# Optimization experiments

Hardware: AMD Instinct MI355X
Metric: run time of the kernel (lower is better)

## Reference

```python
import jax, jax.numpy as jnp
import numpy as np

INPUT_DIM = 8192
OUTPUT_DIM = 16384
SPARSITY = 0.02
TOP_K = int(SPARSITY * OUTPUT_DIM)  # 327


def setup_inputs() -> dict:
    key = jax.random.key(0)
    kx, kp = jax.random.split(key)
    # Binary SDR input, batch of 1 (the layer hard-codes batch=1 in its sparse output)
    x = jax.random.randint(kx, (1, INPUT_DIM), 0, 2, dtype=jnp.int32)
    # Permanence weights ~ U[0, 1), as in tf.random_uniform in build()
    p = jax.random.uniform(kp, (INPUT_DIM, OUTPUT_DIM), dtype=jnp.float32)
    return {"x": x, "p": p}


def reference(x, p):
    # connection = round(permanence) -> binary {0,1} int32 connectivity matrix
    connection = jnp.round(p).astype(jnp.int32)
    # overlap: int32 binarized GEMV, [1, OUTPUT_DIM]
    overlap = jnp.matmul(x, connection)
    # top-k winner columns (unsorted in tf; index set is identical)
    _, act_indices = jax.lax.top_k(overlap[0], TOP_K)
    # Dense equivalent of SparseTensor(indices, ones, [1, OUTPUT_DIM])
    activation = jnp.zeros((1, OUTPUT_DIM), dtype=jnp.float32).at[0, act_indices].set(1.0)
    return activation
```

## Files before the change

### kernel.cpp

```cpp
#include <hip/hip_runtime.h>
#include <hip/hip_bf16.h>

#define IN_DIM 8192
#define OUT_DIM 16384
#define K_TOP 327

__global__ void zero_kernel(int* __restrict__ overlap) {
    int i = blockIdx.x * blockDim.x + threadIdx.x;
    if (i < OUT_DIM) overlap[i] = 0;
}

__global__ __launch_bounds__(256) void overlap_kernel(const int* __restrict__ x,
                                                      const float* __restrict__ p,
                                                      int* __restrict__ overlap) {
    constexpr int ROWS = 128;
    __shared__ int rows[ROWS];
    __shared__ int nact_sh;
    const int tid = threadIdx.x;
    const int row0 = blockIdx.y * ROWS;

    if (tid == 0) nact_sh = 0;
    __syncthreads();
    if (tid < ROWS) {
        if (x[row0 + tid] != 0) {
            int idx = atomicAdd(&nact_sh, 1);
            rows[idx] = tid;
        }
    }
    __syncthreads();
    const int n = nact_sh;

    const int col = blockIdx.x * 1024 + tid * 4;
    const float* pc = p + col;
    int a0 = 0, a1 = 0, a2 = 0, a3 = 0;

    int k = 0;
    for (; k + 1 < n; k += 2) {
        int r1 = rows[k], r2 = rows[k + 1];
        float4 v1 = *(const float4*)(pc + (size_t)(row0 + r1) * OUT_DIM);
        float4 v2 = *(const float4*)(pc + (size_t)(row0 + r2) * OUT_DIM);
        a0 += (v1.x > 0.5f) + (v2.x > 0.5f);
        a1 += (v1.y > 0.5f) + (v2.y > 0.5f);
        a2 += (v1.z > 0.5f) + (v2.z > 0.5f);
        a3 += (v1.w > 0.5f) + (v2.w > 0.5f);
    }
    if (k < n) {
        int r1 = rows[k];
        float4 v1 = *(const float4*)(pc + (size_t)(row0 + r1) * OUT_DIM);
        a0 += (v1.x > 0.5f);
        a1 += (v1.y > 0.5f);
        a2 += (v1.z > 0.5f);
        a3 += (v1.w > 0.5f);
    }
    atomicAdd(&overlap[col + 0], a0);
    atomicAdd(&overlap[col + 1], a1);
    atomicAdd(&overlap[col + 2], a2);
    atomicAdd(&overlap[col + 3], a3);
}

__device__ __forceinline__ int block_scan_incl(int val, int tid, int* wsums) {
    const int lane = tid & 63;
    const int wave = tid >> 6;
    int v = val;
#pragma unroll
    for (int d = 1; d < 64; d <<= 1) {
        int nv = __shfl_up(v, d, 64);
        if (lane >= d) v += nv;
    }
    if (lane == 63) wsums[wave] = v;
    __syncthreads();
    if (wave == 0) {
        int w = (lane < 16) ? wsums[lane] : 0;
#pragma unroll
        for (int d = 1; d < 16; d <<= 1) {
            int nw = __shfl_up(w, d, 64);
            if (lane >= d) w += nw;
        }
        if (lane < 16) wsums[lane] = w;
    }
    __syncthreads();
    int offset = (wave > 0) ? wsums[wave - 1] : 0;
    return v + offset;
}

#define NB 9216
__global__ __launch_bounds__(1024) void topk_kernel(const int* __restrict__ overlap,
                                                    float* __restrict__ out) {
    __shared__ int hist[NB];
    __shared__ int wsums[16];
    __shared__ int sh_T;
    __shared__ int sh_R;
    const int tid = threadIdx.x;

    for (int i = tid; i < NB; i += 1024) hist[i] = 0;
    if (tid == 0) sh_T = -1;
    __syncthreads();

    int ov_local[16];
#pragma unroll
    for (int c = 0; c < 16; ++c) {
        int ov = overlap[c * 1024 + tid];
        ov_local[c] = ov;
        atomicAdd(&hist[ov], 1);
    }
    __syncthreads();

    const int base = tid * 9;
    int h[9];
    int s = 0;
#pragma unroll
    for (int k = 0; k < 9; ++k) {
        h[k] = hist[base + k];
        s += h[k];
    }
    int incl = block_scan_incl(s, tid, wsums);
    int total = wsums[15];
    int suf_excl = total - incl;

    int run = 0;
    int local_T = -1, local_cgt = 0;
#pragma unroll
    for (int k = 8; k >= 0; --k) {
        run += h[k];
        if (local_T < 0 && (suf_excl + run) >= K_TOP) {
            local_T = base + k;
            local_cgt = suf_excl + run - h[k];
        }
    }
    __syncthreads();
    if (local_T >= 0) atomicMax(&sh_T, local_T);
    __syncthreads();
    const int T = sh_T;
    if (local_T == T && local_T >= 0) sh_R = K_TOP - local_cgt;
    __syncthreads();
    const int R = sh_R;

    int running = 0;
#pragma unroll
    for (int c = 0; c < 16; ++c) {
        int ov = ov_local[c];
        int flag = (ov == T) ? 1 : 0;
        int pincl = block_scan_incl(flag, tid, wsums);
        int pexcl = pincl - flag;
        int sel = (ov > T) || (flag && (running + pexcl) < R);
        out[c * 1024 + tid] = sel ? 1.0f : 0.0f;
        running += wsums[15];
        __syncthreads();
    }
}

extern "C" void kernel_launch(void* const* d_in, const int* in_sizes, int n_in,
                              void* d_out, int out_size, void* d_ws, size_t ws_size,
                              hipStream_t stream) {
    const int* x = (const int*)d_in[0];
    const float* p = (const float*)d_in[1];
    float* out = (float*)d_out;
    int* overlap = (int*)d_ws;

    zero_kernel<<<64, 256, 0, stream>>>(overlap);
    overlap_kernel<<<dim3(16, 64), 256, 0, stream>>>(x, p, overlap);
    topk_kernel<<<1, 1024, 0, stream>>>(overlap, out);
}
```

Before: 648.5 us.

## Replace global atomics with per-chunk partials and reduce kernel; nontemporal 4-way loads

The overlap kernel now writes per-row-chunk partial counts to a workspace buffer instead of issuing global atomicAdds, and a new reduce kernel sums the 64 partials per column. This removes the zero kernel and the atomic contention. The inner loop is unrolled to four rows with nontemporal vector loads so more memory requests are in flight and streaming data bypasses the cache. The cost is an extra 4 MB workspace write and read plus another launch.

After: 628.7 us. -3.1%, faster.

```diff
diff --git a/kernel.cpp b/kernel.cpp
--- a/kernel.cpp
+++ b/kernel.cpp
@@ -4,58 +4,64 @@
 #define IN_DIM 8192
 #define OUT_DIM 16384
 #define K_TOP 327
+#define ROW_CHUNKS 64
+#define ROWS_PER_CHUNK 128
 
-__global__ void zero_kernel(int* __restrict__ overlap) {
-    int i = blockIdx.x * blockDim.x + threadIdx.x;
-    if (i < OUT_DIM) overlap[i] = 0;
-}
+typedef float vf4 __attribute__((ext_vector_type(4)));
 
 __global__ __launch_bounds__(256) void overlap_kernel(const int* __restrict__ x,
                                                       const float* __restrict__ p,
-                                                      int* __restrict__ overlap) {
-    constexpr int ROWS = 128;
-    __shared__ int rows[ROWS];
+                                                      int* __restrict__ partial) {
+    __shared__ int rows[ROWS_PER_CHUNK];
     __shared__ int nact_sh;
     const int tid = threadIdx.x;
-    const int row0 = blockIdx.y * ROWS;
+    const int row0 = blockIdx.y * ROWS_PER_CHUNK;
 
     if (tid == 0) nact_sh = 0;
     __syncthreads();
-    if (tid < ROWS) {
+    if (tid < ROWS_PER_CHUNK) {
         if (x[row0 + tid] != 0) {
-            int idx = atomicAdd(&nact_sh, 1);
-            rows[idx] = tid;
+            rows[atomicAdd(&nact_sh, 1)] = tid;
         }
     }
     __syncthreads();
     const int n = nact_sh;
 
     const int col = blockIdx.x * 1024 + tid * 4;
-    const float* pc = p + col;
+    const float* pc = p + (size_t)row0 * OUT_DIM + col;
     int a0 = 0, a1 = 0, a2 = 0, a3 = 0;
 
     int k = 0;
-    for (; k + 1 < n; k += 2) {
-        int r1 = rows[k], r2 = rows[k + 1];
-        float4 v1 = *(const float4*)(pc + (size_t)(row0 + r1) * OUT_DIM);
-        float4 v2 = *(const float4*)(pc + (size_t)(row0 + r2) * OUT_DIM);
-        a0 += (v1.x > 0.5f) + (v2.x > 0.5f);
-        a1 += (v1.y > 0.5f) + (v2.y > 0.5f);
-        a2 += (v1.z > 0.5f) + (v2.z > 0.5f);
-        a3 += (v1.w > 0.5f) + (v2.w > 0.5f);
+    for (; k + 3 < n; k += 4) {
+        int r0 = rows[k], r1 = rows[k + 1], r2 = rows[k + 2], r3 = rows[k + 3];
+        vf4 v0 = __builtin_nontemporal_load((const vf4*)(pc + (size_t)r0 * OUT_DIM));
+        vf4 v1 = __builtin_nontemporal_load((const vf4*)(pc + (size_t)r1 * OUT_DIM));
+        vf4 v2 = __builtin_nontemporal_load((const vf4*)(pc + (size_t)r2 * OUT_DIM));
+        vf4 v3 = __builtin_nontemporal_load((const vf4*)(pc + (size_t)r3 * OUT_DIM));
+        a0 += (v0.x > 0.5f) + (v1.x > 0.5f) + (v2.x > 0.5f) + (v3.x > 0.5f);
+        a1 += (v0.y > 0.5f) + (v1.y > 0.5f) + (v2.y > 0.5f) + (v3.y > 0.5f);
+        a2 += (v0.z > 0.5f) + (v1.z > 0.5f) + (v2.z > 0.5f) + (v3.z > 0.5f);
+        a3 += (v0.w > 0.5f) + (v1.w > 0.5f) + (v2.w > 0.5f) + (v3.w > 0.5f);
     }
-    if (k < n) {
-        int r1 = rows[k];
-        float4 v1 = *(const float4*)(pc + (size_t)(row0 + r1) * OUT_DIM);
-        a0 += (v1.x > 0.5f);
-        a1 += (v1.y > 0.5f);
-        a2 += (v1.z > 0.5f);
-        a3 += (v1.w > 0.5f);
+    for (; k < n; ++k) {
+        int r = rows[k];
+        vf4 v = __builtin_nontemporal_load((const vf4*)(pc + (size_t)r * OUT_DIM));
+        a0 += (v.x > 0.5f);
+        a1 += (v.y > 0.5f);
+        a2 += (v.z > 0.5f);
+        a3 += (v.w > 0.5f);
     }
-    atomicAdd(&overlap[col + 0], a0);
-    atomicAdd(&overlap[col + 1], a1);
-    atomicAdd(&overlap[col + 2], a2);
-    atomicAdd(&overlap[col + 3], a3);
+    int* o = partial + (size_t)blockIdx.y * OUT_DIM + col;
+    o[0] = a0; o[1] = a1; o[2] = a2; o[3] = a3;
+}
+
+__global__ __launch_bounds__(256) void reduce_kernel(const int* __restrict__ partial,
+                                                     int* __restrict__ overlap) {
+    const int t = blockIdx.x * 256 + threadIdx.x;
+    int s = 0;
+#pragma unroll
+    for (int c = 0; c < ROW_CHUNKS; ++c) s += partial[(size_t)c * OUT_DIM + t];
+    overlap[t] = s;
 }
 
 __device__ __forceinline__ int block_scan_incl(int val, int tid, int* wsums) {
@@ -79,8 +85,7 @@
         if (lane < 16) wsums[lane] = w;
     }
     __syncthreads();
-    int offset = (wave > 0) ? wsums[wave - 1] : 0;
-    return v + offset;
+    return v + ((wave > 0) ? wsums[wave - 1] : 0);
 }
 
 #define NB 9216
@@ -155,9 +160,10 @@
     const int* x = (const int*)d_in[0];
     const float* p = (const float*)d_in[1];
     float* out = (float*)d_out;
-    int* overlap = (int*)d_ws;
+    int* partial = (int*)d_ws;
+    int* overlap = (int*)d_ws + ROW_CHUNKS * OUT_DIM;
 
-    zero_kernel<<<64, 256, 0, stream>>>(overlap);
-    overlap_kernel<<<dim3(16, 64), 256, 0, stream>>>(x, p, overlap);
+    overlap_kernel<<<dim3(16, ROW_CHUNKS), 256, 0, stream>>>(x, p, partial);
+    reduce_kernel<<<ROW_CHUNKS, 256, 0, stream>>>(partial, overlap);
     topk_kernel<<<1, 1024, 0, stream>>>(overlap, out);
 }
```
